# Kernel tuning notes

Hardware: AMD Instinct MI355X
Metric: run time of the kernel (lower is better)

## Reference

```python
import jax, jax.numpy as jnp
import numpy as np

N, E, D, H, C = 50000, 1600000, 128, 2, 32

def setup_inputs() -> dict:
    key = jax.random.key(0)
    ks = jax.random.split(key, 8)
    x = jax.random.normal(ks[0], (N, D), jnp.float32)
    edge_index = jax.random.randint(ks[1], (2, E), 0, N)
    intra_enrichment_weights = jax.random.uniform(ks[2], (E,), jnp.float32)
    W = jax.random.normal(ks[3], (D, H * C), jnp.float32) * (1.0 / np.sqrt(D))
    att_src = jax.random.normal(ks[4], (H, C), jnp.float32) * 0.1
    att_dst = jax.random.normal(ks[5], (H, C), jnp.float32) * 0.1
    bias = jnp.zeros((H * C,), jnp.float32)
    enrichment_scale = jnp.asarray(0.01, jnp.float32)
    return dict(x=x, edge_index=edge_index,
                intra_enrichment_weights=intra_enrichment_weights,
                W=W, att_src=att_src, att_dst=att_dst, bias=bias,
                enrichment_scale=enrichment_scale)

def reference(x, edge_index, intra_enrichment_weights, W, att_src, att_dst, bias, enrichment_scale):
    n = x.shape[0]
    xf = jax.nn.elu(x)                       # F.elu on input features
    h = (xf @ W).reshape(n, H, C)            # [N, heads, out]
    # GATConv default add_self_loops=True
    loop = jnp.arange(n, dtype=edge_index.dtype)
    src = jnp.concatenate([edge_index[0], loop])
    dst = jnp.concatenate([edge_index[1], loop])
    a_src = jnp.einsum('nhc,hc->nh', h, att_src)   # [N, H]
    a_dst = jnp.einsum('nhc,hc->nh', h, att_dst)
    alpha = jax.nn.leaky_relu(a_src[src] + a_dst[dst], 0.2)  # [E+N, H]
    # softmax over incoming edges per destination node
    m = jax.ops.segment_max(alpha, dst, num_segments=n)
    e = jnp.exp(alpha - m[dst])
    denom = jax.ops.segment_sum(e, dst, num_segments=n)
    p = e / denom[dst]                       # every node has a self-loop -> denom > 0
    out = jax.ops.segment_sum(h[src] * p[:, :, None], dst, num_segments=n)  # [N, H, C]
    out = out.reshape(n, H * C) + bias
    # enrichment bias (scatter-mean of per-edge weights over source nodes)
    s0 = edge_index[0]
    nw = jax.ops.segment_sum(intra_enrichment_weights, s0, num_segments=n)
    cnt = jax.ops.segment_sum(jnp.ones_like(intra_enrichment_weights), s0, num_segments=n)
    nw = nw / jnp.maximum(cnt, 1.0)
    nw = jnp.clip(nw, 0.2, 5.0)
    scale_factor = 0.1 * jax.nn.sigmoid(enrichment_scale)
    return out + scale_factor * (nw[:, None] - 1.0)
```

## Files before the change

### kernel.cpp

```cpp
#include <hip/hip_runtime.h>


typedef unsigned int u32;
typedef unsigned short u16;

#define SLOTS 4864
#define NB_MAX 400
#define EPB 4096

#define XS 136
#define CS 68

typedef __attribute__((ext_vector_type(8))) short short8;
typedef __attribute__((ext_vector_type(4))) float float4v;

__device__ __forceinline__ u16 f2bf(float f) {
    union { float f; u32 u; } v; v.f = f;
    u32 r = v.u + 0x7fffu + ((v.u >> 16) & 1u);
    return (u16)(r >> 16);
}
__device__ __forceinline__ float bf2f(u16 u) {
    union { u32 i; float f; } v; v.i = ((u32)u) << 16; return v.f;
}
__device__ __forceinline__ float bf_lo(u32 u) {
    union { u32 i; float f; } v; v.i = u << 16; return v.f;
}
__device__ __forceinline__ float bf_hi(u32 u) {
    union { u32 i; float f; } v; v.i = u & 0xFFFF0000u; return v.f;
}
__device__ __forceinline__ void bf_split(float v, short& hi, short& lo) {
    u16 h = f2bf(v);
    float hf = bf2f(h);
    hi = (short)h;
    lo = (short)f2bf(v - hf);
}

__global__ void k_init(int* cursA, int* cursB, int nb) {
    int t = threadIdx.x;
    if (t < nb) { cursA[t] = 0; cursB[t] = 0; }
}

__global__ __launch_bounds__(256) void k_node(
    const float* __restrict__ x, const float* __restrict__ Wm,
    const float* __restrict__ att_s, const float* __restrict__ att_d,
    u32* __restrict__ hb32, float* __restrict__ a_src, float* __restrict__ a_dst,
    int nN)
{
    __shared__ __align__(16) short Ah[64 * XS];
    __shared__ __align__(16) short Al[64 * XS];
    __shared__ __align__(16) short Bh[64 * XS];
    __shared__ __align__(16) short Bl[64 * XS];
    float* Cl = (float*)Ah;

    int t = threadIdx.x;
    int n0 = blockIdx.x * 64;

    {
        int f = t & 63, kq = t >> 6;
        for (int kk = 0; kk < 32; ++kk) {
            int k = kq * 32 + kk;
            float wv = Wm[k * 64 + f];
            short hi, lo; bf_split(wv, hi, lo);
            Bh[f * XS + k] = hi; Bl[f * XS + k] = lo;
        }
    }
    for (int j = 0; j < 8; ++j) {
        int idx = t + 256 * j;
        int r = idx >> 5, c4 = idx & 31;
        int gn = n0 + r;
        float4 xv = make_float4(0.f, 0.f, 0.f, 0.f);
        if (gn < nN) xv = ((const float4*)x)[(size_t)gn * 32 + c4];
        float e[4];
        e[0] = xv.x > 0.f ? xv.x : expm1f(xv.x);
        e[1] = xv.y > 0.f ? xv.y : expm1f(xv.y);
        e[2] = xv.z > 0.f ? xv.z : expm1f(xv.z);
        e[3] = xv.w > 0.f ? xv.w : expm1f(xv.w);
        short h4[4], l4[4];
#pragma unroll
        for (int i = 0; i < 4; ++i) bf_split(e[i], h4[i], l4[i]);
        *(short4*)&Ah[r * XS + c4 * 4] = make_short4(h4[0], h4[1], h4[2], h4[3]);
        *(short4*)&Al[r * XS + c4 * 4] = make_short4(l4[0], l4[1], l4[2], l4[3]);
    }
    __syncthreads();

    {
        int w = t >> 6, l = t & 63;
        int q = l >> 4, m = l & 15;
        int arow = w * 16 + m;
        float4v acc[4] = {};
#pragma unroll
        for (int ks = 0; ks < 4; ++ks) {
            int k0 = ks * 32 + q * 8;
            short8 ah = *(const short8*)&Ah[arow * XS + k0];
            short8 al = *(const short8*)&Al[arow * XS + k0];
#pragma unroll
            for (int nt = 0; nt < 4; ++nt) {
                short8 bh = *(const short8*)&Bh[(nt * 16 + m) * XS + k0];
                short8 bl = *(const short8*)&Bl[(nt * 16 + m) * XS + k0];
                acc[nt] = __builtin_amdgcn_mfma_f32_16x16x32_bf16(ah, bh, acc[nt], 0, 0, 0);
                acc[nt] = __builtin_amdgcn_mfma_f32_16x16x32_bf16(ah, bl, acc[nt], 0, 0, 0);
                acc[nt] = __builtin_amdgcn_mfma_f32_16x16x32_bf16(al, bh, acc[nt], 0, 0, 0);
            }
        }
        __syncthreads();
#pragma unroll
        for (int nt = 0; nt < 4; ++nt)
#pragma unroll
            for (int r = 0; r < 4; ++r)
                Cl[(w * 16 + q * 4 + r) * CS + nt * 16 + m] = acc[nt][r];
    }
    __syncthreads();

    {
        int nl = t >> 2, fq = t & 3;
        int gn = n0 + nl;
        float ps = 0.f, pd = 0.f;
        if (gn < nN) {
            float hv[16];
#pragma unroll
            for (int i = 0; i < 16; ++i) {
                int f = fq * 16 + i;
                hv[i] = Cl[nl * CS + f];
                ps = fmaf(hv[i], att_s[f], ps);
                pd = fmaf(hv[i], att_d[f], pd);
            }
#pragma unroll
            for (int i = 0; i < 8; ++i) {
                u32 pk = ((u32)f2bf(hv[2 * i + 1]) << 16) | (u32)f2bf(hv[2 * i]);
                hb32[(size_t)gn * 32 + fq * 8 + i] = pk;
            }
        }
        float ps2 = ps + __shfl_xor(ps, 1, 64);
        float pd2 = pd + __shfl_xor(pd, 1, 64);
        if (gn < nN && (fq & 1) == 0) {
            a_src[2 * gn + (fq >> 1)] = ps2;
            a_dst[2 * gn + (fq >> 1)] = pd2;
        }
    }
}

__global__ __launch_bounds__(256) void k_partA(
    const int* __restrict__ ei, const float* __restrict__ wgt,
    int* cursA, int* cursB, u32* bufA, u32* bufB, int E, int nb)
{
    __shared__ u32 arrA[EPB], arrB[EPB];
    __shared__ u16 bkA[EPB], bkB[EPB];
    __shared__ int cntA[NB_MAX], cntB[NB_MAX];
    __shared__ int lofsA[NB_MAX], lofsB[NB_MAX];
    __shared__ int basA[NB_MAX], basB[NB_MAX];
    __shared__ int part[256];

    int t = threadIdx.x;
    for (int b = t; b < nb; b += 256) { cntA[b] = 0; cntB[b] = 0; }
    __syncthreads();

    int base = blockIdx.x * EPB;
    int nv = min(EPB, E - base);
    int sv[16], dv[16]; float wv[16];
#pragma unroll
    for (int k = 0; k < 16; ++k) {
        int e = base + k * 256 + t;
        if (e < E) { sv[k] = ei[e]; dv[k] = ei[E + e]; wv[k] = wgt[e]; }
        else       { sv[k] = -1;    dv[k] = -1;        wv[k] = 0.f; }
    }
#pragma unroll
    for (int k = 0; k < 16; ++k) {
        if (dv[k] >= 0) {
            atomicAdd(&cntA[dv[k] >> 7], 1);
            atomicAdd(&cntB[sv[k] >> 7], 1);
        }
    }
    __syncthreads();
    for (int b = t; b < nb; b += 256) {
        int ca = cntA[b], cb = cntB[b];
        if (ca > 0) basA[b] = atomicAdd(&cursA[b], ca);
        if (cb > 0) basB[b] = atomicAdd(&cursB[b], cb);
    }
    __syncthreads();
    {
        int b0 = 2 * t, b1 = 2 * t + 1;
        int c0 = (b0 < nb) ? cntA[b0] : 0;
        int c1 = (b1 < nb) ? cntA[b1] : 0;
        part[t] = c0 + c1;
        __syncthreads();
        for (int off = 1; off < 256; off <<= 1) {
            int v = (t >= off) ? part[t - off] : 0;
            __syncthreads();
            part[t] += v;
            __syncthreads();
        }
        int excl = part[t] - (c0 + c1);
        if (b0 < nb) lofsA[b0] = excl;
        if (b1 < nb) lofsA[b1] = excl + c0;
        __syncthreads();
        c0 = (b0 < nb) ? cntB[b0] : 0;
        c1 = (b1 < nb) ? cntB[b1] : 0;
        part[t] = c0 + c1;
        __syncthreads();
        for (int off = 1; off < 256; off <<= 1) {
            int v = (t >= off) ? part[t - off] : 0;
            __syncthreads();
            part[t] += v;
            __syncthreads();
        }
        excl = part[t] - (c0 + c1);
        if (b0 < nb) lofsB[b0] = excl;
        if (b1 < nb) lofsB[b1] = excl + c0;
    }
    __syncthreads();
    for (int b = t; b < nb; b += 256) { cntA[b] = 0; cntB[b] = 0; }
    __syncthreads();
#pragma unroll
    for (int k = 0; k < 16; ++k) {
        if (dv[k] >= 0) {
            int bA = dv[k] >> 7;
            int r = lofsA[bA] + atomicAdd(&cntA[bA], 1);
            arrA[r] = ((u32)(dv[k] & 127) << 16) | (u32)sv[k];
            bkA[r] = (u16)bA;
            int bB = sv[k] >> 7;
            u32 wf = (u32)(wv[k] * 16777216.f);
            if (wf > 0xFFFFFFu) wf = 0xFFFFFFu;
            int r2 = lofsB[bB] + atomicAdd(&cntB[bB], 1);
            arrB[r2] = ((u32)(sv[k] & 127) << 24) | wf;
            bkB[r2] = (u16)bB;
        }
    }
    __syncthreads();
    for (int i = t; i < nv; i += 256) {
        int bA = bkA[i];
        int g = basA[bA] + (i - lofsA[bA]);
        if (g < SLOTS) bufA[bA * SLOTS + g] = arrA[i];
    }
    for (int i = t; i < nv; i += 256) {
        int bB = bkB[i];
        int g = basB[bB] + (i - lofsB[bB]);
        if (g < SLOTS) bufB[bB * SLOTS + g] = arrB[i];
    }
}

__global__ __launch_bounds__(256) void k_partB_dst(
    const u32* bufA_in, const int* __restrict__ cursA,
    u32* bufA_out, int* __restrict__ deg, int* __restrict__ offs, int nN)
{
    __shared__ u32 st[SLOTS];
    __shared__ u32 st2[SLOTS];
    __shared__ int ldeg[128], lscan[128], lcur[128];
    int b = blockIdx.x, t = threadIdx.x;
    int n = cursA[b]; if (n > SLOTS) n = SLOTS;
    if (t < 128) { ldeg[t] = 0; lcur[t] = 0; }
    __syncthreads();
    for (int i = t; i < n; i += 256) {
        u32 v = bufA_in[b * SLOTS + i];
        st[i] = v;
        atomicAdd(&ldeg[v >> 16], 1);
    }
    __syncthreads();
    if (t < 128) lscan[t] = ldeg[t];
    __syncthreads();
    for (int off = 1; off < 128; off <<= 1) {
        int v = 0;
        if (t < 128 && t >= off) v = lscan[t - off];
        __syncthreads();
        if (t < 128) lscan[t] += v;
        __syncthreads();
    }
    int excl = 0;
    if (t < 128) excl = lscan[t] - ldeg[t];
    __syncthreads();
    if (t < 128) lscan[t] = excl;
    __syncthreads();
    for (int i = t; i < n; i += 256) {
        u32 v = st[i];
        int dl = v >> 16;
        int pos = lscan[dl] + atomicAdd(&lcur[dl], 1);
        st2[pos] = v & 0xFFFFu;
    }
    __syncthreads();
    for (int i = t; i < n; i += 256) bufA_out[b * SLOTS + i] = st2[i];
    int node = (b << 7) + t;
    if (t < 128 && node < nN) { deg[node] = ldeg[t]; offs[node] = b * SLOTS + lscan[t]; }
}

__global__ __launch_bounds__(256) void k_partB_src(
    const u32* __restrict__ bufB, const int* __restrict__ cursB,
    float* __restrict__ nwv, int nN)
{
    __shared__ u32 usum[128]; __shared__ int ucnt[128];
    int b = blockIdx.x, t = threadIdx.x;
    int n = cursB[b]; if (n > SLOTS) n = SLOTS;
    if (t < 128) { usum[t] = 0; ucnt[t] = 0; }
    __syncthreads();
    for (int i = t; i < n; i += 256) {
        u32 v = bufB[b * SLOTS + i];
        atomicAdd(&usum[v >> 24], v & 0xFFFFFFu);
        atomicAdd(&ucnt[v >> 24], 1);
    }
    __syncthreads();
    int node = (b << 7) + t;
    if (t < 128 && node < nN) {
        float cnt = (float)ucnt[t];
        float nw = ((float)usum[t] * (1.f / 16777216.f)) / fmaxf(cnt, 1.f);
        nwv[node] = fminf(fmaxf(nw, 0.2f), 5.f);
    }
}

__global__ __launch_bounds__(256) void k_accum(
    const u32* __restrict__ hb32,
    const float* __restrict__ a_src, const float* __restrict__ a_dst,
    const u32* __restrict__ esrc, const int* __restrict__ offs,
    const int* __restrict__ deg, const float* __restrict__ nwv,
    const float* __restrict__ bias, const float* __restrict__ esc,
    float* __restrict__ out, int nN)
{
    __shared__ u32 lds[4][2][64][2];
    int tid = threadIdx.x;
    int lane = tid & 63;
    int n = (blockIdx.x * 256 + tid) >> 6;
    if (n >= nN) return;
    int ws = tid >> 6;
    int l31 = lane & 31;
    int half = lane >> 5;
    int head = l31 >> 4;

    float ad0 = a_dst[2 * n], ad1 = a_dst[2 * n + 1];
    float as0 = a_src[2 * n], as1 = a_src[2 * n + 1];
    float t0 = as0 + ad0; t0 = t0 > 0.f ? t0 : 0.2f * t0;
    float t1 = as1 + ad1; t1 = t1 > 0.f ? t1 : 0.2f * t1;
    float es0 = __expf(t0), es1 = __expf(t1);

    u32 hself = hb32[(size_t)n * 32 + l31];
    float eself = head ? es1 : es0;
    float acc0 = half ? 0.f : eself * bf_lo(hself);
    float acc1 = half ? 0.f : eself * bf_hi(hself);
    float dsum0 = 0.f, dsum1 = 0.f;

    int start = offs[n], len = deg[n];
    for (int b0 = 0; b0 < len; b0 += 64) {
        int cnt = min(64, len - b0);
        u32 si = (u32)n; float e0 = 0.f, e1 = 0.f;
        if (lane < cnt) {
            si = esrc[start + b0 + lane];
            float2 ap = ((const float2*)a_src)[si];
            float v0 = ap.x + ad0; v0 = v0 > 0.f ? v0 : 0.2f * v0;
            float v1 = ap.y + ad1; v1 = v1 > 0.f ? v1 : 0.2f * v1;
            e0 = __expf(v0); e1 = __expf(v1);
        }
        dsum0 += e0; dsum1 += e1;
        lds[ws][0][lane][0] = si; lds[ws][0][lane][1] = __float_as_uint(e0);
        lds[ws][1][lane][0] = si; lds[ws][1][lane][1] = __float_as_uint(e1);

        int iters = (cnt + 1) >> 1;
#pragma unroll 4
        for (int k = 0; k < iters; ++k) {
            int e = 2 * k + half;
            u32 rsi = lds[ws][head][e][0];
            float w = __uint_as_float(lds[ws][head][e][1]);
            u32 hv = hb32[(size_t)rsi * 32 + l31];
            acc0 = fmaf(w, bf_lo(hv), acc0);
            acc1 = fmaf(w, bf_hi(hv), acc1);
        }
    }

#pragma unroll
    for (int off = 1; off < 64; off <<= 1) {
        dsum0 += __shfl_xor(dsum0, off, 64);
        dsum1 += __shfl_xor(dsum1, off, 64);
    }
    float den0 = es0 + dsum0, den1 = es1 + dsum1;

    acc0 += __shfl_xor(acc0, 32, 64);
    acc1 += __shfl_xor(acc1, 32, 64);

    if (half == 0) {
        float den = head ? den1 : den0;
        float sf = 0.1f / (1.f + __expf(-esc[0]));
        float en = sf * (nwv[n] - 1.f);
        float2 bb = ((const float2*)bias)[l31];
        float2 o;
        o.x = acc0 / den + bb.x + en;
        o.y = acc1 / den + bb.y + en;
        ((float2*)out)[(size_t)n * 32 + l31] = o;
    }
}

extern "C" void kernel_launch(void* const* d_in, const int* in_sizes, int n_in,
                              void* d_out, int out_size, void* d_ws, size_t ws_size,
                              hipStream_t stream)
{
    const float* x     = (const float*)d_in[0];
    const int*   ei    = (const int*)d_in[1];
    const float* wgt   = (const float*)d_in[2];
    const float* Wm    = (const float*)d_in[3];
    const float* att_s = (const float*)d_in[4];
    const float* att_d = (const float*)d_in[5];
    const float* bias  = (const float*)d_in[6];
    const float* esc   = (const float*)d_in[7];
    float* out = (float*)d_out;

    int nN = in_sizes[0] / 128;
    int E  = in_sizes[2];
    int NB = (nN + 127) / 128;

    char* p = (char*)d_ws;
    auto alloc = [&](size_t bytes) -> char* {
        char* r = p; p += (bytes + 255) & ~(size_t)255; return r;
    };
    u32*   hb32  = (u32*)  alloc((size_t)nN * 32 * 4);
    float* a_src = (float*)alloc((size_t)nN * 2 * 4);
    float* a_dst = (float*)alloc((size_t)nN * 2 * 4);
    int*   deg   = (int*)  alloc((size_t)nN * 4);
    int*   offs  = (int*)  alloc((size_t)nN * 4);
    float* nwv   = (float*)alloc((size_t)nN * 4);
    int*   cursA = (int*)  alloc(NB_MAX * 4);
    int*   cursB = (int*)  alloc(NB_MAX * 4);
    u32*   bufA  = (u32*)  alloc((size_t)NB * SLOTS * 4);
    u32*   bufB  = (u32*)  alloc((size_t)NB * SLOTS * 4);

    int nblkA = (E + EPB - 1) / EPB;

    k_init<<<dim3(1), dim3(512), 0, stream>>>(cursA, cursB, NB);
    k_node<<<dim3((nN + 63) / 64), dim3(256), 0, stream>>>(x, Wm, att_s, att_d, hb32, a_src, a_dst, nN);
    k_partA<<<dim3(nblkA), dim3(256), 0, stream>>>(ei, wgt, cursA, cursB, bufA, bufB, E, NB);
    k_partB_dst<<<dim3(NB), dim3(256), 0, stream>>>(bufA, cursA, bufA, deg, offs, nN);
    k_partB_src<<<dim3(NB), dim3(256), 0, stream>>>(bufB, cursB, nwv, nN);
    k_accum<<<dim3((nN + 3) / 4), dim3(256), 0, stream>>>(hb32, a_src, a_dst, bufA, offs, deg,
                                                          nwv, bias, esc, out, nN);
}
```

Measured before the change: 191.6 us.

## Fuse partB kernels and widen accumulate gathers to 8-byte loads

Merges the dst-bucket sort kernel and the src enrichment-mean kernel into one launch, so each block handles both buffers and one launch is saved. In the accumulate kernel each lane now gathers a uint2 (4 bf16 features) instead of a u32, which lets four edges be processed in parallel per wavefront (quarter-wave groups) rather than two. The per-edge weights are stored as a float2 in LDS, and the final reduction uses two cross-lane shuffles. The fused kernel uses more LDS per block, and the wider gathers give fewer but larger memory requests, plus extra shuffle work at the end.

```diff
diff --git a/kernel.cpp b/kernel.cpp
--- a/kernel.cpp
+++ b/kernel.cpp
@@ -238,22 +238,31 @@
     }
 }
 
-__global__ __launch_bounds__(256) void k_partB_dst(
+__global__ __launch_bounds__(256) void k_partB(
     const u32* bufA_in, const int* __restrict__ cursA,
-    u32* bufA_out, int* __restrict__ deg, int* __restrict__ offs, int nN)
+    u32* bufA_out, int* __restrict__ deg, int* __restrict__ offs,
+    const u32* __restrict__ bufB, const int* __restrict__ cursB,
+    float* __restrict__ nwv, int nN)
 {
     __shared__ u32 st[SLOTS];
     __shared__ u32 st2[SLOTS];
     __shared__ int ldeg[128], lscan[128], lcur[128];
+    __shared__ u32 usum[128]; __shared__ int ucnt[128];
     int b = blockIdx.x, t = threadIdx.x;
-    int n = cursA[b]; if (n > SLOTS) n = SLOTS;
-    if (t < 128) { ldeg[t] = 0; lcur[t] = 0; }
-    __syncthreads();
-    for (int i = t; i < n; i += 256) {
+    int nA = cursA[b]; if (nA > SLOTS) nA = SLOTS;
+    int nB = cursB[b]; if (nB > SLOTS) nB = SLOTS;
+    if (t < 128) { ldeg[t] = 0; lcur[t] = 0; usum[t] = 0; ucnt[t] = 0; }
+    __syncthreads();
+    for (int i = t; i < nA; i += 256) {
         u32 v = bufA_in[b * SLOTS + i];
         st[i] = v;
         atomicAdd(&ldeg[v >> 16], 1);
     }
+    for (int i = t; i < nB; i += 256) {
+        u32 v = bufB[b * SLOTS + i];
+        atomicAdd(&usum[v >> 24], v & 0xFFFFFFu);
+        atomicAdd(&ucnt[v >> 24], 1);
+    }
     __syncthreads();
     if (t < 128) lscan[t] = ldeg[t];
     __syncthreads();
@@ -269,35 +278,18 @@
     __syncthreads();
     if (t < 128) lscan[t] = excl;
     __syncthreads();
-    for (int i = t; i < n; i += 256) {
+    for (int i = t; i < nA; i += 256) {
         u32 v = st[i];
         int dl = v >> 16;
         int pos = lscan[dl] + atomicAdd(&lcur[dl], 1);
         st2[pos] = v & 0xFFFFu;
     }
     __syncthreads();
-    for (int i = t; i < n; i += 256) bufA_out[b * SLOTS + i] = st2[i];
-    int node = (b << 7) + t;
-    if (t < 128 && node < nN) { deg[node] = ldeg[t]; offs[node] = b * SLOTS + lscan[t]; }
-}
-
-__global__ __launch_bounds__(256) void k_partB_src(
-    const u32* __restrict__ bufB, const int* __restrict__ cursB,
-    float* __restrict__ nwv, int nN)
-{
-    __shared__ u32 usum[128]; __shared__ int ucnt[128];
-    int b = blockIdx.x, t = threadIdx.x;
-    int n = cursB[b]; if (n > SLOTS) n = SLOTS;
-    if (t < 128) { usum[t] = 0; ucnt[t] = 0; }
-    __syncthreads();
-    for (int i = t; i < n; i += 256) {
-        u32 v = bufB[b * SLOTS + i];
-        atomicAdd(&usum[v >> 24], v & 0xFFFFFFu);
-        atomicAdd(&ucnt[v >> 24], 1);
-    }
-    __syncthreads();
+    for (int i = t; i < nA; i += 256) bufA_out[b * SLOTS + i] = st2[i];
     int node = (b << 7) + t;
     if (t < 128 && node < nN) {
+        deg[node] = ldeg[t];
+        offs[node] = b * SLOTS + lscan[t];
         float cnt = (float)ucnt[t];
         float nw = ((float)usum[t] * (1.f / 16777216.f)) / fmaxf(cnt, 1.f);
         nwv[node] = fminf(fmaxf(nw, 0.2f), 5.f);
@@ -312,15 +304,16 @@
     const float* __restrict__ bias, const float* __restrict__ esc,
     float* __restrict__ out, int nN)
 {
-    __shared__ u32 lds[4][2][64][2];
+    __shared__ u32    lds_si[4][64];
+    __shared__ float2 lds_w[4][64];
     int tid = threadIdx.x;
     int lane = tid & 63;
     int n = (blockIdx.x * 256 + tid) >> 6;
     if (n >= nN) return;
     int ws = tid >> 6;
-    int l31 = lane & 31;
-    int half = lane >> 5;
-    int head = l31 >> 4;
+    int q  = lane >> 4;
+    int fl = lane & 15;
+    int head = fl >> 3;
 
     float ad0 = a_dst[2 * n], ad1 = a_dst[2 * n + 1];
     float as0 = a_src[2 * n], as1 = a_src[2 * n + 1];
@@ -328,10 +321,16 @@
     float t1 = as1 + ad1; t1 = t1 > 0.f ? t1 : 0.2f * t1;
     float es0 = __expf(t0), es1 = __expf(t1);
 
-    u32 hself = hb32[(size_t)n * 32 + l31];
-    float eself = head ? es1 : es0;
-    float acc0 = half ? 0.f : eself * bf_lo(hself);
-    float acc1 = half ? 0.f : eself * bf_hi(hself);
+    const uint2* hb2 = (const uint2*)hb32;
+    float acc0 = 0.f, acc1 = 0.f, acc2 = 0.f, acc3 = 0.f;
+    if (q == 0) {
+        uint2 hs = hb2[(size_t)n * 16 + fl];
+        float eself = head ? es1 : es0;
+        acc0 = eself * bf_lo(hs.x);
+        acc1 = eself * bf_hi(hs.x);
+        acc2 = eself * bf_lo(hs.y);
+        acc3 = eself * bf_hi(hs.y);
+    }
     float dsum0 = 0.f, dsum1 = 0.f;
 
     int start = offs[n], len = deg[n];
@@ -346,18 +345,21 @@
             e0 = __expf(v0); e1 = __expf(v1);
         }
         dsum0 += e0; dsum1 += e1;
-        lds[ws][0][lane][0] = si; lds[ws][0][lane][1] = __float_as_uint(e0);
-        lds[ws][1][lane][0] = si; lds[ws][1][lane][1] = __float_as_uint(e1);
-
-        int iters = (cnt + 1) >> 1;
-#pragma unroll 4
+        lds_si[ws][lane] = si;
+        lds_w[ws][lane]  = make_float2(e0, e1);
+
+        int iters = (cnt + 3) >> 2;
+#pragma unroll 8
         for (int k = 0; k < iters; ++k) {
-            int e = 2 * k + half;
-            u32 rsi = lds[ws][head][e][0];
-            float w = __uint_as_float(lds[ws][head][e][1]);
-            u32 hv = hb32[(size_t)rsi * 32 + l31];
-            acc0 = fmaf(w, bf_lo(hv), acc0);
-            acc1 = fmaf(w, bf_hi(hv), acc1);
+            int e = 4 * k + q;
+            u32 rsi = lds_si[ws][e];
+            float2 w2 = lds_w[ws][e];
+            float w = head ? w2.y : w2.x;
+            uint2 hv = hb2[(size_t)rsi * 16 + fl];
+            acc0 = fmaf(w, bf_lo(hv.x), acc0);
+            acc1 = fmaf(w, bf_hi(hv.x), acc1);
+            acc2 = fmaf(w, bf_lo(hv.y), acc2);
+            acc3 = fmaf(w, bf_hi(hv.y), acc3);
         }
     }
 
@@ -368,18 +370,22 @@
     }
     float den0 = es0 + dsum0, den1 = es1 + dsum1;
 
-    acc0 += __shfl_xor(acc0, 32, 64);
-    acc1 += __shfl_xor(acc1, 32, 64);
-
-    if (half == 0) {
+    acc0 += __shfl_xor(acc0, 16, 64); acc0 += __shfl_xor(acc0, 32, 64);
+    acc1 += __shfl_xor(acc1, 16, 64); acc1 += __shfl_xor(acc1, 32, 64);
+    acc2 += __shfl_xor(acc2, 16, 64); acc2 += __shfl_xor(acc2, 32, 64);
+    acc3 += __shfl_xor(acc3, 16, 64); acc3 += __shfl_xor(acc3, 32, 64);
+
+    if (q == 0) {
         float den = head ? den1 : den0;
         float sf = 0.1f / (1.f + __expf(-esc[0]));
         float en = sf * (nwv[n] - 1.f);
-        float2 bb = ((const float2*)bias)[l31];
-        float2 o;
+        float4 bb = ((const float4*)bias)[fl];
+        float4 o;
         o.x = acc0 / den + bb.x + en;
         o.y = acc1 / den + bb.y + en;
-        ((float2*)out)[(size_t)n * 32 + l31] = o;
+        o.z = acc2 / den + bb.z + en;
+        o.w = acc3 / den + bb.w + en;
+        ((float4*)out)[(size_t)n * 16 + fl] = o;
     }
 }
 
@@ -421,8 +427,7 @@
     k_init<<<dim3(1), dim3(512), 0, stream>>>(cursA, cursB, NB);
     k_node<<<dim3((nN + 63) / 64), dim3(256), 0, stream>>>(x, Wm, att_s, att_d, hb32, a_src, a_dst, nN);
     k_partA<<<dim3(nblkA), dim3(256), 0, stream>>>(ei, wgt, cursA, cursB, bufA, bufB, E, NB);
-    k_partB_dst<<<dim3(NB), dim3(256), 0, stream>>>(bufA, cursA, bufA, deg, offs, nN);
-    k_partB_src<<<dim3(NB), dim3(256), 0, stream>>>(bufB, cursB, nwv, nN);
+    k_partB<<<dim3(NB), dim3(256), 0, stream>>>(bufA, cursA, bufA, deg, offs, bufB, cursB, nwv, nN);
     k_accum<<<dim3((nN + 3) / 4), dim3(256), 0, stream>>>(hb32, a_src, a_dst, bufA, offs, deg,
                                                           nwv, bias, esc, out, nN);
 }
```

Measured after the change: 190.6 us. Within noise of the previous version (-0.5%).
